# Performance work log

Measured on AMD Instinct MI355X. Metric: run time of the kernel, lower is better.

## Reference

```python
import jax, jax.numpy as jnp
import numpy as np

MAP_SHAPE = (40, 50)   # SOM grid -> L = 2000 landmarks
NUM_FEATURE = 64
BATCH = 2048
R = 1.0
GAMMA = 1.0 / (2.0 * R ** 2)


def _make_qd():
    # Pairwise squared distances between 2D grid coordinates, Gaussian kernel.
    ii, jj = np.meshgrid(np.arange(MAP_SHAPE[0]), np.arange(MAP_SHAPE[1]), indexing='ij')
    coords = np.stack([ii.ravel(), jj.ravel()], axis=1).astype(np.float32)  # (L, 2)
    d2 = ((coords[:, None, :] - coords[None, :, :]) ** 2).sum(-1)           # (L, L)
    return jnp.asarray(np.exp(-GAMMA * d2), dtype=jnp.float32)


def setup_inputs() -> dict:
    key = jax.random.key(0)
    kx, kl = jax.random.split(key)
    x = jax.random.normal(kx, (BATCH, NUM_FEATURE), dtype=jnp.float32)
    landmarks = jax.random.normal(kl, (MAP_SHAPE[0] * MAP_SHAPE[1], NUM_FEATURE), dtype=jnp.float32)
    qd = _make_qd()
    return {"x": x, "landmarks": landmarks, "qd": qd}


def reference(x, landmarks, qd):
    # Squared Euclidean distances: (B, L)
    xlm = x @ landmarks.T
    x2 = jnp.sum(jnp.square(x), axis=1, keepdims=True)        # (B, 1)
    lm2 = jnp.sum(jnp.square(landmarks), axis=1)               # (L,)
    d = x2 + lm2 - 2.0 * xlm                                   # (B, L)
    min_idx = jnp.argmin(d, axis=-1)                            # (B,) BMU index
    h = qd[min_idx]                                             # (B, L) neighborhood weights
    # delta0[b, l, f] = h[b, l] * (x[b, f] - landmarks[l, f])
    delta0 = h[:, :, None] * (x[:, None, :] - landmarks[None, :, :])  # (B, L, F)
    return delta0
```

## Files before the change

### kernel.cpp

```cpp
#include <hip/hip_runtime.h>

#define L_LM 2000
#define F_DIM 64
#define B_SZ 2048

typedef float f32x4 __attribute__((ext_vector_type(4)));

__global__ __launch_bounds__(256) void som_bmu_kernel(
    const float* __restrict__ x, const float* __restrict__ lm,
    int* __restrict__ min_idx)
{
    constexpr int ROWS = 8;
    const int b0 = blockIdx.x * ROWS;
    const int tid = threadIdx.x;

    __shared__ float xs[ROWS][F_DIM];
    for (int i = tid; i < ROWS * F_DIM; i += 256) {
        xs[i / F_DIM][i % F_DIM] = x[(size_t)(b0 + i / F_DIM) * F_DIM + (i % F_DIM)];
    }
    __syncthreads();

    float best[ROWS];
    int   bidx[ROWS];
#pragma unroll
    for (int r = 0; r < ROWS; ++r) { best[r] = 3.4e38f; bidx[r] = 0; }

    for (int l = tid; l < L_LM; l += 256) {
        const float4* lp = reinterpret_cast<const float4*>(lm + (size_t)l * F_DIM);
        float dot[ROWS];
        float l2 = 0.f;
#pragma unroll
        for (int r = 0; r < ROWS; ++r) dot[r] = 0.f;
#pragma unroll
        for (int k = 0; k < F_DIM / 4; ++k) {
            float4 v = lp[k];
            l2 += v.x * v.x + v.y * v.y + v.z * v.z + v.w * v.w;
#pragma unroll
            for (int r = 0; r < ROWS; ++r) {
                dot[r] += v.x * xs[r][4 * k + 0] + v.y * xs[r][4 * k + 1]
                        + v.z * xs[r][4 * k + 2] + v.w * xs[r][4 * k + 3];
            }
        }
#pragma unroll
        for (int r = 0; r < ROWS; ++r) {
            float s = l2 - 2.f * dot[r];
            if (s < best[r]) { best[r] = s; bidx[r] = l; }
        }
    }

#pragma unroll
    for (int r = 0; r < ROWS; ++r) {
        float s = best[r]; int i = bidx[r];
        for (int off = 32; off > 0; off >>= 1) {
            float s2 = __shfl_down(s, off);
            int   i2 = __shfl_down(i, off);
            if (s2 < s || (s2 == s && i2 < i)) { s = s2; i = i2; }
        }
        best[r] = s; bidx[r] = i;
    }

    __shared__ float sbest[4][ROWS];
    __shared__ int   sidx[4][ROWS];
    const int wave = tid >> 6;
    const int lane = tid & 63;
    if (lane == 0) {
#pragma unroll
        for (int r = 0; r < ROWS; ++r) { sbest[wave][r] = best[r]; sidx[wave][r] = bidx[r]; }
    }
    __syncthreads();
    if (tid < ROWS) {
        float s = sbest[0][tid]; int i = sidx[0][tid];
#pragma unroll
        for (int w = 1; w < 4; ++w) {
            float s2 = sbest[w][tid]; int i2 = sidx[w][tid];
            if (s2 < s || (s2 == s && i2 < i)) { s = s2; i = i2; }
        }
        min_idx[b0 + tid] = i;
    }
}

__global__ __launch_bounds__(256) void som_delta_kernel(
    const float* __restrict__ x, const float* __restrict__ lm,
    const float* __restrict__ qd, const int* __restrict__ min_idx,
    f32x4* __restrict__ out)
{
    constexpr int ROW4 = L_LM * F_DIM / 4;
    const int b = blockIdx.x;
    const int tid = threadIdx.x;

    const int bmu = min_idx[b];
    const float* __restrict__ qrow = qd + (size_t)bmu * L_LM;
    const f32x4 xv = reinterpret_cast<const f32x4*>(x + (size_t)b * F_DIM)[tid & 15];
    const f32x4* __restrict__ lmv = reinterpret_cast<const f32x4*>(lm);
    f32x4* __restrict__ ob = out + (size_t)b * ROW4;

#pragma unroll 5
    for (int i = tid; i < ROW4; i += 256) {
        const int l = i >> 4;
        const float h = qrow[l];
        const f32x4 lv = lmv[i];
        f32x4 o;
        o.x = h * (xv.x - lv.x);
        o.y = h * (xv.y - lv.y);
        o.z = h * (xv.z - lv.z);
        o.w = h * (xv.w - lv.w);
        __builtin_nontemporal_store(o, &ob[i]);
    }
}

extern "C" void kernel_launch(void* const* d_in, const int* in_sizes, int n_in,
                              void* d_out, int out_size, void* d_ws, size_t ws_size,
                              hipStream_t stream) {
    const float* x  = (const float*)d_in[0];
    const float* lm = (const float*)d_in[1];
    const float* qd = (const float*)d_in[2];
    float* out = (float*)d_out;
    int* midx = (int*)d_ws;

    som_bmu_kernel<<<B_SZ / 8, 256, 0, stream>>>(x, lm, midx);

    som_delta_kernel<<<B_SZ, 256, 0, stream>>>(x, lm, qd, midx, (f32x4*)out);
}
```

Before: 280.2 us.

## Tile delta kernel over landmark and batch blocks to reuse landmark data

Restructures the delta kernel into 2D tiles of 16 landmarks by 128 batch rows. Each block loads its landmark slice once into registers and stages x rows and neighbourhood weights in shared memory. This removes the repeated per-row reads of the whole landmark matrix. In exchange, output writes become 4 KB strided chunks across rows instead of long contiguous rows, and there is extra shared-memory staging and synchronisation.

```diff
diff --git a/kernel.cpp b/kernel.cpp
--- a/kernel.cpp
+++ b/kernel.cpp
@@ -3,6 +3,8 @@
 #define L_LM 2000
 #define F_DIM 64
 #define B_SZ 2048
+#define CL 16
+#define CB 128
 
 typedef float f32x4 __attribute__((ext_vector_type(4)));
 
@@ -82,29 +84,47 @@
 __global__ __launch_bounds__(256) void som_delta_kernel(
     const float* __restrict__ x, const float* __restrict__ lm,
     const float* __restrict__ qd, const int* __restrict__ min_idx,
-    f32x4* __restrict__ out)
+    float* __restrict__ out)
 {
-    constexpr int ROW4 = L_LM * F_DIM / 4;
-    const int b = blockIdx.x;
+    const int l0 = blockIdx.x * CL;
+    const int b0 = blockIdx.y * CB;
     const int tid = threadIdx.x;
+    const int f4 = tid & 15;
+    const int lg = tid >> 4;
 
-    const int bmu = min_idx[b];
-    const float* __restrict__ qrow = qd + (size_t)bmu * L_LM;
-    const f32x4 xv = reinterpret_cast<const f32x4*>(x + (size_t)b * F_DIM)[tid & 15];
-    const f32x4* __restrict__ lmv = reinterpret_cast<const f32x4*>(lm);
-    f32x4* __restrict__ ob = out + (size_t)b * ROW4;
+    __shared__ float xs[CB][F_DIM];
+    __shared__ float hs[CB][CL];
+    __shared__ int   bmu[CB];
 
-#pragma unroll 5
-    for (int i = tid; i < ROW4; i += 256) {
-        const int l = i >> 4;
-        const float h = qrow[l];
-        const f32x4 lv = lmv[i];
+    {
+        const f32x4* src = reinterpret_cast<const f32x4*>(x + (size_t)b0 * F_DIM);
+        f32x4* dst = reinterpret_cast<f32x4*>(&xs[0][0]);
+        for (int i = tid; i < CB * F_DIM / 4; i += 256) dst[i] = src[i];
+    }
+    if (tid < CB) bmu[tid] = min_idx[b0 + tid];
+
+    const f32x4 lv = reinterpret_cast<const f32x4*>(lm + (size_t)(l0 + lg) * F_DIM)[f4];
+
+    __syncthreads();
+
+    for (int i = tid; i < CB * CL; i += 256) {
+        const int b = i >> 4, j = i & 15;
+        hs[b][j] = qd[(size_t)bmu[b] * L_LM + l0 + j];
+    }
+    __syncthreads();
+
+    float* ob = out + (size_t)b0 * (L_LM * F_DIM) + (size_t)l0 * F_DIM;
+#pragma unroll 4
+    for (int b = 0; b < CB; ++b) {
+        const float h = hs[b][lg];
+        const f32x4 xv = reinterpret_cast<const f32x4*>(&xs[b][0])[f4];
         f32x4 o;
         o.x = h * (xv.x - lv.x);
         o.y = h * (xv.y - lv.y);
         o.z = h * (xv.z - lv.z);
         o.w = h * (xv.w - lv.w);
-        __builtin_nontemporal_store(o, &ob[i]);
+        __builtin_nontemporal_store(
+            o, reinterpret_cast<f32x4*>(ob + (size_t)b * (L_LM * F_DIM)) + tid);
     }
 }
 
@@ -119,5 +139,6 @@
 
     som_bmu_kernel<<<B_SZ / 8, 256, 0, stream>>>(x, lm, midx);
 
-    som_delta_kernel<<<B_SZ, 256, 0, stream>>>(x, lm, qd, midx, (f32x4*)out);
+    dim3 grid(L_LM / CL, B_SZ / CB);
+    som_delta_kernel<<<grid, 256, 0, stream>>>(x, lm, qd, midx, out);
 }
```

Result: faster. 261.1 us (-6.8%).
